# Optimization experiments

Hardware: AMD Instinct MI355X
Metric: run time of the kernel (lower is better)

The kernel has to match this reference:

```python
import jax, jax.numpy as jnp
import numpy as np

EPS = 1e-6
LAMB = 0.05
NEG = -1000.0


def setup_inputs() -> dict:
    key = jax.random.key(0)
    k1, k2, k3, k4, k5, k6 = jax.random.split(key, 6)
    Bi, Bt, K, L, D = 128, 128, 36, 64, 1024
    imgs = jax.random.normal(k1, (Bi, K, D), dtype=jnp.float32)
    caps = jax.random.normal(k2, (Bt, L, D), dtype=jnp.float32)
    img_cls = jax.random.normal(k3, (Bi, D), dtype=jnp.float32)
    cap_cls = jax.random.normal(k4, (Bt, D), dtype=jnp.float32)
    # variable lengths; pin one element to max so torch's [:, :max] slice is identity
    img_lens = jax.random.randint(k5, (Bi,), K // 2, K + 1).astype(jnp.int32).at[0].set(K)
    cap_lens = jax.random.randint(k6, (Bt,), L // 2, L + 1).astype(jnp.int32).at[0].set(L)
    return {"img_cls": img_cls, "imgs": imgs, "cap_cls": cap_cls,
            "caps": caps, "img_lens": img_lens, "cap_lens": cap_lens}


def reference(img_cls, imgs, cap_cls, caps, img_lens, cap_lens):
    # HiCHAN.forward_cam (img_cls / cap_cls unused by this branch)
    imgs = imgs + EPS
    caps = caps + EPS
    imgs = imgs / jnp.linalg.norm(imgs, axis=-1, keepdims=True)
    caps = caps / jnp.linalg.norm(caps, axis=-1, keepdims=True)

    K, L = imgs.shape[1], caps.shape[1]
    # fine-grained similarity tensor [Bi, Bt, K, L]
    fg_sims = jnp.einsum('ikd,tld->itkl', imgs, caps)

    # fg mask: valid region k of image i AND valid word l of caption t
    img_valid = jnp.arange(K)[None, :] < img_lens[:, None]      # [Bi, K]
    cap_valid = jnp.arange(L)[None, :] < cap_lens[:, None]      # [Bt, L]
    mask = img_valid[:, None, :, None] & cap_valid[None, :, None, :]  # [Bi,Bt,K,L] bool
    m = mask.astype(fg_sims.dtype)

    # masked temperature softmax (single scores tensor reused for both axes)
    scores = jnp.where(mask, fg_sims, NEG) / LAMB
    v2t_attn = jax.nn.softmax(scores, axis=-1)
    v2t = jnp.sum(v2t_attn * fg_sims * m, axis=-1)   # [Bi,Bt,K]
    t2v_attn = jax.nn.softmax(scores, axis=-2)
    t2v = jnp.sum(t2v_attn * fg_sims * m, axis=-2)   # [Bi,Bt,L]

    # _ave_init: uniform weights over valid rows / cols
    r_b = mask.any(axis=-1).astype(fg_sims.dtype)    # [Bi,Bt,K]
    c_b = mask.any(axis=-2).astype(fg_sims.dtype)    # [Bi,Bt,L]
    r = r_b / r_b.sum(axis=-1, keepdims=True)
    c = c_b / c_b.sum(axis=-1, keepdims=True)

    sims = (jnp.sum(v2t * r, axis=-1) + jnp.sum(t2v * c, axis=-1)) / 2  # [Bi,Bt]
    return sims
```

## Files before the change

### kernel.cpp

```cpp
#include <hip/hip_runtime.h>
#include <stdint.h>

#define BI 128
#define BT 128
#define KIMG 36
#define LCAP 64
#define DD 1024
#define MP 48
#define MB 96
#define NB 256
#define ABUF 6144

typedef _Float16 h4 __attribute__((ext_vector_type(4)));
typedef _Float16 h8 __attribute__((ext_vector_type(8)));
typedef float f4 __attribute__((ext_vector_type(4)));

__device__ __forceinline__ float wave_red_sum(float v) {
#pragma unroll
  for (int o = 1; o < 64; o <<= 1) v += __shfl_xor(v, o, 64);
  return v;
}
__device__ __forceinline__ float wave_red_max(float v) {
#pragma unroll
  for (int o = 1; o < 64; o <<= 1) v = fmaxf(v, __shfl_xor(v, o, 64));
  return v;
}

__global__ __launch_bounds__(256) void norm_kernel(
    const float* __restrict__ imgs, const float* __restrict__ caps,
    _Float16* __restrict__ Ah, _Float16* __restrict__ Bh) {
  int row = blockIdx.x;
  int tid = threadIdx.x;
  const float* src;
  bool isCap;
  int r = 0;
  if (row < BI * MP) {
    int i = row / MP, k = row - i * MP;
    isCap = false;
    if (k >= KIMG) {
      h4 z = {};
      ((h4*)(Ah + (size_t)row * DD))[tid] = z;
      return;
    }
    src = imgs + ((size_t)i * KIMG + k) * DD;
  } else {
    r = row - BI * MP;
    isCap = true;
    src = caps + (size_t)r * DD;
  }
  float4 x = ((const float4*)src)[tid];
  x.x += 1e-6f; x.y += 1e-6f; x.z += 1e-6f; x.w += 1e-6f;
  float ss = x.x * x.x + x.y * x.y + x.z * x.z + x.w * x.w;
  ss = wave_red_sum(ss);
  __shared__ float red[4];
  int lane = tid & 63, w = tid >> 6;
  if (lane == 0) red[w] = ss;
  __syncthreads();
  float scale = rsqrtf(red[0] + red[1] + red[2] + red[3]);
  h4 o;
  o[0] = (_Float16)(x.x * scale);
  o[1] = (_Float16)(x.y * scale);
  o[2] = (_Float16)(x.z * scale);
  o[3] = (_Float16)(x.w * scale);
  if (!isCap) {
    ((h4*)(Ah + (size_t)row * DD))[tid] = o;
  } else {
    int k = 4 * tid;
    size_t tile = (size_t)(r >> 4) * 32 + (k >> 5);
    int sub = ((k >> 3) & 3) * 128 + (r & 15) * 8 + (k & 7);
    *(h4*)(Bh + tile * 512 + sub) = o;
  }
}

__global__ __launch_bounds__(256, 3) void sims_kernel(
    const _Float16* __restrict__ Ah, const _Float16* __restrict__ Bh,
    const int* __restrict__ img_lens, const int* __restrict__ cap_lens,
    float* __restrict__ out) {
  __shared__ char stage[2 * ABUF] __attribute__((aligned(16)));

  int tid = threadIdx.x;
  int lane = tid & 63;
  int w = tid >> 6;

  int wgid = blockIdx.x;
  int xcd = wgid & 7;
  int slot = wgid >> 3;
  int bx = 4 * xcd + (slot & 3);
  int by = slot >> 2;

  int fr = lane & 15;
  int fq = lane >> 4;

  const size_t arow0 = (size_t)by * MB;
  const size_t brow0 = (size_t)bx * NB;

  const int c0 = (w < 2) ? 2 * w : w + 2;
  const int nch = (w < 2) ? 2 : 1;
  int s0 = c0 * 64 + lane;
  int sw0 = s0 ^ ((s0 >> 3) & 7);
  const _Float16* gpA = Ah + (arow0 + (sw0 >> 2)) * DD + (sw0 & 3) * 8;
  const int lds0 = c0 * 1024 + lane * 16;

  int sl = 4 * fr + fq;
  const int aoff0 = (sl ^ ((sl >> 3) & 7)) * 16;

  const _Float16* bp[4];
#pragma unroll
  for (int ni = 0; ni < 4; ++ni)
    bp[ni] = Bh + ((size_t)((bx * 16) + 4 * w + ni) * 32) * 512 + lane * 8;

  f4 acc[6][4] = {};
  h8 bfA[4], bfB[4];

  auto STAGE = [&](int buf, int k0) {
    __builtin_amdgcn_global_load_lds(
        (const __attribute__((address_space(1))) void*)(gpA + k0),
        (__attribute__((address_space(3))) void*)(stage + buf * ABUF + lds0), 16, 0, 0);
    if (nch == 2)
      __builtin_amdgcn_global_load_lds(
          (const __attribute__((address_space(1))) void*)(gpA + 16 * DD + k0),
          (__attribute__((address_space(3))) void*)(stage + buf * ABUF + lds0 + 1024), 16, 0, 0);
  };
  auto LOADB = [&](h8(&bf)[4], int t) {
#pragma unroll
    for (int ni = 0; ni < 4; ++ni) bf[ni] = *(const h8*)(bp[ni] + 512 * t);
  };
  auto BODY = [&](int t, int parity, h8(&cur)[4], h8(&nxt)[4]) {
    if (t < 31) {
      STAGE(parity ^ 1, 32 * (t + 1));
      LOADB(nxt, t + 1);
    }
    const char* rb = stage + parity * ABUF;
    h8 af[6];
#pragma unroll
    for (int mi = 0; mi < 6; ++mi)
      af[mi] = *(const h8*)(rb + aoff0 + 1024 * mi);
    __builtin_amdgcn_s_setprio(1);
#pragma unroll
    for (int mi = 0; mi < 6; ++mi)
#pragma unroll
      for (int ni = 0; ni < 4; ++ni)
        acc[mi][ni] = __builtin_amdgcn_mfma_f32_16x16x32_f16(
            af[mi], cur[ni], acc[mi][ni], 0, 0, 0);
    __builtin_amdgcn_s_setprio(0);
    __syncthreads();
  };

  STAGE(0, 0);
  LOADB(bfA, 0);
  __syncthreads();

  for (int tt = 0; tt < 32; tt += 2) {
    BODY(tt, 0, bfA, bfB);
    BODY(tt + 1, 1, bfB, bfA);
  }

  int t = bx * 4 + w;
  int Lt = cap_lens[t];

#pragma unroll
  for (int img = 0; img < 2; ++img) {
    int Ki = img_lens[2 * by + img];

    float m = -1e30f;
#pragma unroll
    for (int mi = 0; mi < 3; ++mi)
#pragma unroll
      for (int ni = 0; ni < 4; ++ni)
#pragma unroll
        for (int j = 0; j < 4; ++j) {
          bool valid = (16 * mi + 4 * fq + j < Ki) && (16 * ni + fr < Lt);
          if (valid) m = fmaxf(m, acc[3 * img + mi][ni][j]);
        }
    m = wave_red_max(m);

    float rowe[3][4] = {}, rowes[3][4] = {}, cole[4] = {}, coles[4] = {};
#pragma unroll
    for (int mi = 0; mi < 3; ++mi)
#pragma unroll
      for (int ni = 0; ni < 4; ++ni)
#pragma unroll
        for (int j = 0; j < 4; ++j) {
          float s = acc[3 * img + mi][ni][j];
          bool valid = (16 * mi + 4 * fq + j < Ki) && (16 * ni + fr < Lt);
          float e = valid ? __expf((s - m) * 20.0f) : 0.f;
          float es = e * s;
          rowe[mi][j] += e;
          rowes[mi][j] += es;
          cole[ni] += e;
          coles[ni] += es;
        }

    float part = 0.f;
#pragma unroll
    for (int mi = 0; mi < 3; ++mi)
#pragma unroll
      for (int j = 0; j < 4; ++j) {
        float Re = rowe[mi][j], Res = rowes[mi][j];
#pragma unroll
        for (int o = 1; o < 16; o <<= 1) {
          Re += __shfl_xor(Re, o, 64);
          Res += __shfl_xor(Res, o, 64);
        }
        int row = 16 * mi + 4 * fq + j;
        if (fr == 0 && row < Ki) part += (Res / Re) * (0.5f / (float)Ki);
      }
#pragma unroll
    for (int ni = 0; ni < 4; ++ni) {
      float Ce = cole[ni], Ces = coles[ni];
#pragma unroll
      for (int o = 16; o < 64; o <<= 1) {
        Ce += __shfl_xor(Ce, o, 64);
        Ces += __shfl_xor(Ces, o, 64);
      }
      int l = 16 * ni + fr;
      if (fq == 0 && l < Lt) part += (Ces / Ce) * (0.5f / (float)Lt);
    }
    float sim = wave_red_sum(part);
    if (lane == 0) out[(size_t)(2 * by + img) * BT + t] = sim;
  }
}

extern "C" void kernel_launch(void* const* d_in, const int* in_sizes, int n_in,
                              void* d_out, int out_size, void* d_ws, size_t ws_size,
                              hipStream_t stream) {
  const float* imgs = (const float*)d_in[1];
  const float* caps = (const float*)d_in[3];
  const int* img_lens = (const int*)d_in[4];
  const int* cap_lens = (const int*)d_in[5];
  float* out = (float*)d_out;

  _Float16* Ah = (_Float16*)d_ws;
  _Float16* Bh = Ah + (size_t)BI * MP * DD;

  norm_kernel<<<BI * MP + BT * LCAP, 256, 0, stream>>>(imgs, caps, Ah, Bh);
  sims_kernel<<<2048, 256, 0, stream>>>(Ah, Bh, img_lens, cap_lens, out);
}
```

Baseline: 141.2 us.

## Deepen B-operand prefetch to two steps with triple register buffering

The GEMM main loop now prefetches B fragments two k-steps ahead, rotating through three register buffers, while A tiles still double-buffer in LDS. The full __syncthreads is replaced by an explicit s_waitcnt vmcnt(4) plus s_barrier, so the newest B loads can stay in flight across the barrier. The loop is unrolled by six with a peeled tail. The aim is to hide global-load latency of B behind the MFMA work, at the cost of extra VGPRs under a 3-waves-per-SIMD launch bound.

```diff
diff --git a/kernel.cpp b/kernel.cpp
--- a/kernel.cpp
+++ b/kernel.cpp
@@ -92,7 +92,6 @@
   int fq = lane >> 4;
 
   const size_t arow0 = (size_t)by * MB;
-  const size_t brow0 = (size_t)bx * NB;
 
   const int c0 = (w < 2) ? 2 * w : w + 2;
   const int nch = (w < 2) ? 2 : 1;
@@ -110,7 +109,7 @@
     bp[ni] = Bh + ((size_t)((bx * 16) + 4 * w + ni) * 32) * 512 + lane * 8;
 
   f4 acc[6][4] = {};
-  h8 bfA[4], bfB[4];
+  h8 bfA[4], bfB[4], bfC[4];
 
   auto STAGE = [&](int buf, int k0) {
     __builtin_amdgcn_global_load_lds(
@@ -125,11 +124,7 @@
 #pragma unroll
     for (int ni = 0; ni < 4; ++ni) bf[ni] = *(const h8*)(bp[ni] + 512 * t);
   };
-  auto BODY = [&](int t, int parity, h8(&cur)[4], h8(&nxt)[4]) {
-    if (t < 31) {
-      STAGE(parity ^ 1, 32 * (t + 1));
-      LOADB(nxt, t + 1);
-    }
+  auto COMPUTE = [&](int parity, h8(&cur)[4]) {
     const char* rb = stage + parity * ABUF;
     h8 af[6];
 #pragma unroll
@@ -143,17 +138,37 @@
         acc[mi][ni] = __builtin_amdgcn_mfma_f32_16x16x32_f16(
             af[mi], cur[ni], acc[mi][ni], 0, 0, 0);
     __builtin_amdgcn_s_setprio(0);
-    __syncthreads();
+  };
+  auto BODY = [&](int t, h8(&cur)[4], h8(&nxt2)[4]) {
+    STAGE((t + 1) & 1, 32 * (t + 1));
+    LOADB(nxt2, t + 2);
+    COMPUTE(t & 1, cur);
+    asm volatile("s_waitcnt vmcnt(4)" ::: "memory");
+    __builtin_amdgcn_s_barrier();
+    __builtin_amdgcn_sched_barrier(0);
   };
 
   STAGE(0, 0);
   LOADB(bfA, 0);
-  __syncthreads();
-
-  for (int tt = 0; tt < 32; tt += 2) {
-    BODY(tt, 0, bfA, bfB);
-    BODY(tt + 1, 1, bfB, bfA);
-  }
+  LOADB(bfB, 1);
+  asm volatile("s_waitcnt vmcnt(4)" ::: "memory");
+  __builtin_amdgcn_s_barrier();
+  __builtin_amdgcn_sched_barrier(0);
+
+  for (int tt = 0; tt < 30; tt += 6) {
+    BODY(tt + 0, bfA, bfC);
+    BODY(tt + 1, bfB, bfA);
+    BODY(tt + 2, bfC, bfB);
+    BODY(tt + 3, bfA, bfC);
+    BODY(tt + 4, bfB, bfA);
+    BODY(tt + 5, bfC, bfB);
+  }
+  STAGE(1, 32 * 31);
+  COMPUTE(0, bfA);
+  asm volatile("s_waitcnt vmcnt(0)" ::: "memory");
+  __builtin_amdgcn_s_barrier();
+  __builtin_amdgcn_sched_barrier(0);
+  COMPUTE(1, bfB);
 
   int t = bx * 4 + w;
   int Lt = cap_lens[t];
```

New measurement: 477.3 us. 3.38x slower.
